# Performance work log

Hardware: AMD Instinct MI355X
Metric: run time of the kernel (lower is better)

The kernel has to match this reference:

```python
import jax, jax.numpy as jnp
import numpy as np

N = 100000   # n_entity
D = 128      # kg_emb_dim
R = 12       # n_relation
NB = 8       # num_bases
E = 1_000_000
P = 400_000  # hypergraph incidences
HE = 20_000  # hyperedges
B = 64       # users in batch
LR = 64      # related entities per hypergraph per user
LC = 32      # context entities per user
NH = 8       # mha heads
HD = D // NH


def setup_inputs() -> dict:
    key = jax.random.key(0)
    ks = jax.random.split(key, 32)
    s = 1.0 / np.sqrt(D)
    f = lambda i, shape, sc=s: jax.random.normal(ks[i], shape, dtype=jnp.float32) * sc
    ri = lambda i, shape, hi: jax.random.randint(ks[i], shape, 0, hi, dtype=jnp.int32)
    return {
        'entity_emb': f(0, (N, D)),
        'rgcn_bases': f(1, (NB, D, D)),
        'rgcn_comp': f(2, (R, NB)),
        'rgcn_root': f(3, (D, D)),
        'rgcn_bias': jnp.zeros((D,), jnp.float32),
        'sess_theta': f(4, (D, D)),
        'sess_bias': jnp.zeros((D,), jnp.float32),
        'know_theta': f(5, (D, D)),
        'know_bias': jnp.zeros((D,), jnp.float32),
        'in_proj_w': f(6, (3 * D, D)),
        'in_proj_b': jnp.zeros((3 * D,), jnp.float32),
        'out_proj_w': f(7, (D, D)),
        'out_proj_b': jnp.zeros((D,), jnp.float32),
        'attn_his_a': f(8, (D, D)),
        'attn_his_b': f(9, (D, 1)),
        'attn_a': f(10, (D, D)),
        'attn_b': f(11, (D, 1)),
        'rec_bias': jnp.zeros((N,), jnp.float32),
        'edge_src': ri(12, (E,), N),
        'edge_dst': ri(13, (E,), N),
        'edge_type': ri(14, (E,), R),
        'sess_nodes': ri(15, (P,), N),
        'sess_edges': ri(16, (P,), HE),
        'know_nodes': ri(17, (P,), N),
        'know_edges': ri(18, (P,), HE),
        'sess_rel_idx': ri(19, (B, LR), N),
        'know_rel_idx': ri(20, (B, LR), N),
        'context_idx': ri(21, (B, LC), N),
    }


def rgcn_conv(x, bases, comp, root, bias, src, dst, etype):
    # PyG RGCNConv with basis decomposition; per-relation mean aggregation
    # norm = 1/|N_r(i)| : count edges per (dst, relation)
    pair_key = dst * R + etype
    cnt = jax.ops.segment_sum(jnp.ones_like(src, dtype=x.dtype), pair_key, N * R)
    norm = 1.0 / jnp.maximum(cnt[pair_key], 1.0)  # [E]
    w = jnp.einsum('rb,bio->rio', comp, bases)    # [R, D, D]
    out = x @ root + bias
    for r in range(R):
        h_r = x @ w[r]                                            # [N, D]
        coef = norm * (etype == r).astype(x.dtype)                # [E]
        out = out + jax.ops.segment_sum(h_r[src] * coef[:, None], dst, N)
    return out


def hypergraph_conv(x, theta, bias, nodes, edges, n_hyperedges):
    # PyG HypergraphConv (no attention): D^-1 H W B^-1 H^T X Theta + bias
    xt = x @ theta                                                # [N, D]
    ones = jnp.ones(nodes.shape, x.dtype)
    b_deg = jax.ops.segment_sum(ones, edges, n_hyperedges)        # [HE]
    edge_feat = jax.ops.segment_sum(xt[nodes], edges, n_hyperedges)
    edge_feat = edge_feat * jnp.where(b_deg > 0, 1.0 / b_deg, 0.0)[:, None]
    d_deg = jax.ops.segment_sum(ones, nodes, N)                   # [N]
    out = jax.ops.segment_sum(edge_feat[edges], nodes, N)
    return out * jnp.where(d_deg > 0, 1.0 / d_deg, 0.0)[:, None] + bias


def self_attn_batch(h, a, b):
    # SelfAttentionBatch: e = tanh(h a) b; softmax over nodes; weighted sum
    e = jnp.einsum('bld,dk->blk', jnp.tanh(jnp.einsum('bld,de->ble', h, a)), b)[..., 0]
    attn = jax.nn.softmax(e, axis=-1)                             # [B, L]
    return jnp.einsum('bl,bld->bd', attn, h)


def mha(q, kv, in_proj_w, in_proj_b, out_proj_w, out_proj_b):
    # torch.nn.MultiheadAttention (batch_first) math
    wq, wk, wv = in_proj_w[:D], in_proj_w[D:2 * D], in_proj_w[2 * D:]
    bq, bk, bv = in_proj_b[:D], in_proj_b[D:2 * D], in_proj_b[2 * D:]
    qh = (q @ wq.T + bq).reshape(q.shape[0], q.shape[1], NH, HD)
    kh = (kv @ wk.T + bk).reshape(kv.shape[0], kv.shape[1], NH, HD)
    vh = (kv @ wv.T + bv).reshape(kv.shape[0], kv.shape[1], NH, HD)
    logits = jnp.einsum('bqhd,bkhd->bhqk', qh, kh) / np.sqrt(HD)
    attn = jax.nn.softmax(logits, axis=-1)
    o = jnp.einsum('bhqk,bkhd->bqhd', attn, vh).reshape(q.shape[0], q.shape[1], D)
    return o @ out_proj_w.T + out_proj_b


def reference(entity_emb, rgcn_bases, rgcn_comp, rgcn_root, rgcn_bias,
              sess_theta, sess_bias, know_theta, know_bias,
              in_proj_w, in_proj_b, out_proj_w, out_proj_b,
              attn_his_a, attn_his_b, attn_a, attn_b, rec_bias,
              edge_src, edge_dst, edge_type,
              sess_nodes, sess_edges, know_nodes, know_edges,
              sess_rel_idx, know_rel_idx, context_idx):
    # 1) RGCN over the full KG
    kg = rgcn_conv(entity_emb, rgcn_bases, rgcn_comp, rgcn_root, rgcn_bias,
                   edge_src, edge_dst, edge_type)
    # 2) session / knowledge hypergraph convolutions on RGCN output
    sess = hypergraph_conv(kg, sess_theta, sess_bias, sess_nodes, sess_edges, HE)
    know = hypergraph_conv(kg, know_theta, know_bias, know_nodes, know_edges, HE)
    # 3) per-user: related = concat(session_emb, knowledge_emb); context from kg
    related = jnp.concatenate([sess[sess_rel_idx], know[know_rel_idx]], axis=1)  # [B, 2LR, D]
    context = kg[context_idx]                                                    # [B, LC, D]
    # 4) MHItemAttention (context queries related) + gated attention pooling
    att_rel = mha(context, related, in_proj_w, in_proj_b, out_proj_w, out_proj_b)
    his = self_attn_batch(att_rel, attn_his_a, attn_his_b)                       # [B, D]
    user_cat = jnp.concatenate([context, his[:, None, :]], axis=1)               # [B, LC+1, D]
    user = self_attn_batch(user_cat, attn_a, attn_b)                             # [B, D]
    # 5) recommendation scores: F.linear(user, kg_embedding, rec_bias.bias)
    return user @ kg.T + rec_bias                                                # [B, N]
```

## Files before the change

kernel.cpp:

```cpp
#include <hip/hip_runtime.h>
#include <hip/hip_bf16.h>

#define DN 100000
#define DD 128
#define DR 12
#define DNB 8
#define DE 1000000
#define DP 400000
#define DHE 20000
#define DHE2 40000
#define DB 64
#define DLR 64
#define DLC 32
#define DNH 8
#define DHD 16
#define NRBINS (DR * DN)
#define NALLBINS (NRBINS + DHE2)
#define SCAN_CHUNK 1024
#define MCAP 65536

typedef unsigned short ushortT;
typedef unsigned int uintT;
typedef __attribute__((ext_vector_type(8))) short s8v;
typedef __attribute__((ext_vector_type(4))) float f4v;

#define APAD 136
#define ASLB 40
#define BSP 40

__device__ __forceinline__ ushortT rneb(float v) {
    uintT b = __float_as_uint(v);
    return (ushortT)((b + 0x7FFFu + ((b >> 16) & 1u)) >> 16);
}
__device__ __forceinline__ float b2f(ushortT h) {
    return __uint_as_float(((uintT)h) << 16);
}

__device__ __forceinline__ void split_store8(ushortT* hbase, ushortT* lbase, const float* v)
{
    ushortT h[8], l[8];
    #pragma unroll
    for (int j = 0; j < 8; ++j) {
        h[j] = rneb(v[j]);
        l[j] = rneb(v[j] - b2f(h[j]));
    }
    uint4 hv = make_uint4((uintT)h[0] | ((uintT)h[1] << 16), (uintT)h[2] | ((uintT)h[3] << 16),
                          (uintT)h[4] | ((uintT)h[5] << 16), (uintT)h[6] | ((uintT)h[7] << 16));
    uint4 lv = make_uint4((uintT)l[0] | ((uintT)l[1] << 16), (uintT)l[2] | ((uintT)l[3] << 16),
                          (uintT)l[4] | ((uintT)l[5] << 16), (uintT)l[6] | ((uintT)l[7] << 16));
    *(uint4*)hbase = hv;
    *(uint4*)lbase = lv;
}

__global__ __launch_bounds__(256) void k_presplit_all(
    const float* __restrict__ root, const float* __restrict__ st,
    const float* __restrict__ kt, const float* __restrict__ ipw,
    const float* __restrict__ opw, const float* __restrict__ aha,
    const float* __restrict__ aa, ushortT* __restrict__ outA)
{
    int gid = blockIdx.x * 256 + threadIdx.x;
    int mat = gid >> 14, e = gid & 16383;
    const float* srcs[9] = {root, st, kt, ipw, ipw + 16384, ipw + 32768, opw, aha, aa};
    const float* W = srcs[mat];
    bool t1 = (mat >= 3 && mat <= 6);
    int k = e & 31, n = (e >> 5) & 127, kc = e >> 12;
    float f = t1 ? W[(size_t)n * 128 + kc * 32 + k] : W[(size_t)(kc * 32 + k) * 128 + n];
    ushortT h = rneb(f);
    outA[(size_t)mat * 32768 + e] = h;
    outA[(size_t)mat * 32768 + 16384 + e] = rneb(f - b2f(h));
}

__global__ void k_wcomp_split(const float* __restrict__ comp, const float* __restrict__ bases,
                              ushortT* __restrict__ warena)
{
    int i = blockIdx.x * blockDim.x + threadIdx.x;
    if (i >= DR * DD * DD) return;
    int r = i / (DD * DD), io = i % (DD * DD);
    float s = 0.f;
    #pragma unroll
    for (int b = 0; b < DNB; ++b) s += comp[r * DNB + b] * bases[(size_t)b * DD * DD + io];
    int irow = io >> 7, o = io & 127;
    int kc = irow >> 5, k = irow & 31;
    size_t dst = (size_t)r * 32768 + (size_t)kc * 4096 + o * 32 + k;
    ushortT h = rneb(s);
    warena[dst] = h;
    warena[dst + 16384] = rneb(s - b2f(h));
}

__global__ __launch_bounds__(256) void k_gemm_ds(
    const float* __restrict__ A, const ushortT* __restrict__ Wb,
    const float* __restrict__ bias, const float* __restrict__ rs,
    const int* __restrict__ gidx, float* __restrict__ gout,
    float* __restrict__ C, int M)
{
    __shared__ __align__(16) ushortT Ah[64 * APAD], Al[64 * APAD];
    __shared__ __align__(16) ushortT Bs[8192];
    int tid = threadIdx.x;
    int row0 = blockIdx.x * 64;
    {
        int row = tid >> 2, c0 = (tid & 3) * 32;
        int gr = row0 + row;
        int arow = gr;
        if (gidx && gr < M) arow = gidx[gr];
        const float* ar = A + (size_t)arow * 128 + c0;
        float sc = 1.0f;
        if (rs && gr < M) { float d = rs[gr]; sc = (d > 0.f) ? 1.0f / d : 0.f; }
        #pragma unroll
        for (int g = 0; g < 4; ++g) {
            float v[8] = {};
            if (gr < M) {
                float4 u0 = *(const float4*)(ar + g * 8);
                float4 u1 = *(const float4*)(ar + g * 8 + 4);
                v[0]=u0.x*sc; v[1]=u0.y*sc; v[2]=u0.z*sc; v[3]=u0.w*sc;
                v[4]=u1.x*sc; v[5]=u1.y*sc; v[6]=u1.z*sc; v[7]=u1.w*sc;
                if (gout) {
                    *(float4*)(gout + (size_t)gr * 128 + c0 + g * 8)     = u0;
                    *(float4*)(gout + (size_t)gr * 128 + c0 + g * 8 + 4) = u1;
                }
            }
            split_store8(&Ah[row * APAD + c0 + g * 8], &Al[row * APAD + c0 + g * 8], v);
        }
    }
    f4v acc[8] = {};
    int w = tid >> 6, lane = tid & 63, m = lane & 15, quad = lane >> 4;
    for (int kc = 0; kc < 4; ++kc) {
        __syncthreads();
        {
            const ushortT* gh = Wb + kc * 4096;
            const ushortT* gl = Wb + 16384 + kc * 4096;
            *(s8v*)&Bs[tid * 8]        = *(const s8v*)&gh[tid * 8];
            *(s8v*)&Bs[2048 + tid * 8] = *(const s8v*)&gh[2048 + tid * 8];
            *(s8v*)&Bs[4096 + tid * 8] = *(const s8v*)&gl[tid * 8];
            *(s8v*)&Bs[6144 + tid * 8] = *(const s8v*)&gl[2048 + tid * 8];
        }
        __syncthreads();
        s8v ah = *(const s8v*)&Ah[(w * 16 + m) * APAD + kc * 32 + quad * 8];
        s8v al = *(const s8v*)&Al[(w * 16 + m) * APAD + kc * 32 + quad * 8];
        #pragma unroll
        for (int nt = 0; nt < 8; ++nt) {
            int boff = (nt * 16 + m) * 32 + quad * 8;
            s8v bh = *(const s8v*)&Bs[boff];
            s8v bl = *(const s8v*)&Bs[4096 + boff];
            acc[nt] = __builtin_amdgcn_mfma_f32_16x16x32_bf16(ah, bh, acc[nt], 0, 0, 0);
            acc[nt] = __builtin_amdgcn_mfma_f32_16x16x32_bf16(al, bh, acc[nt], 0, 0, 0);
            acc[nt] = __builtin_amdgcn_mfma_f32_16x16x32_bf16(ah, bl, acc[nt], 0, 0, 0);
        }
    }
    float bv[8];
    #pragma unroll
    for (int nt = 0; nt < 8; ++nt) bv[nt] = bias ? bias[nt * 16 + m] : 0.f;
    #pragma unroll
    for (int rr = 0; rr < 4; ++rr) {
        int gr = row0 + w * 16 + quad * 4 + rr;
        if (gr < M) {
            #pragma unroll
            for (int nt = 0; nt < 8; ++nt)
                C[(size_t)gr * 128 + nt * 16 + m] = acc[nt][rr] + bv[nt];
        }
    }
}

__global__ __launch_bounds__(256) void k_tanh_dot_ds(
    const float* __restrict__ A, const ushortT* __restrict__ Wb,
    const float* __restrict__ bvec, float* __restrict__ e, int M)
{
    __shared__ __align__(16) ushortT Ah[64 * APAD], Al[64 * APAD];
    __shared__ __align__(16) ushortT Bs[8192];
    int tid = threadIdx.x;
    int row0 = blockIdx.x * 64;
    {
        int row = tid >> 2, c0 = (tid & 3) * 32;
        int gr = row0 + row;
        const float* ar = A + (size_t)gr * 128 + c0;
        #pragma unroll
        for (int g = 0; g < 4; ++g) {
            float v[8] = {};
            if (gr < M) {
                float4 u0 = *(const float4*)(ar + g * 8);
                float4 u1 = *(const float4*)(ar + g * 8 + 4);
                v[0]=u0.x; v[1]=u0.y; v[2]=u0.z; v[3]=u0.w;
                v[4]=u1.x; v[5]=u1.y; v[6]=u1.z; v[7]=u1.w;
            }
            split_store8(&Ah[row * APAD + c0 + g * 8], &Al[row * APAD + c0 + g * 8], v);
        }
    }
    f4v acc[8] = {};
    int w = tid >> 6, lane = tid & 63, m = lane & 15, quad = lane >> 4;
    for (int kc = 0; kc < 4; ++kc) {
        __syncthreads();
        {
            const ushortT* gh = Wb + kc * 4096;
            const ushortT* gl = Wb + 16384 + kc * 4096;
            *(s8v*)&Bs[tid * 8]        = *(const s8v*)&gh[tid * 8];
            *(s8v*)&Bs[2048 + tid * 8] = *(const s8v*)&gh[2048 + tid * 8];
            *(s8v*)&Bs[4096 + tid * 8] = *(const s8v*)&gl[tid * 8];
            *(s8v*)&Bs[6144 + tid * 8] = *(const s8v*)&gl[2048 + tid * 8];
        }
        __syncthreads();
        s8v ah = *(const s8v*)&Ah[(w * 16 + m) * APAD + kc * 32 + quad * 8];
        s8v al = *(const s8v*)&Al[(w * 16 + m) * APAD + kc * 32 + quad * 8];
        #pragma unroll
        for (int nt = 0; nt < 8; ++nt) {
            int boff = (nt * 16 + m) * 32 + quad * 8;
            s8v bh = *(const s8v*)&Bs[boff];
            s8v bl = *(const s8v*)&Bs[4096 + boff];
            acc[nt] = __builtin_amdgcn_mfma_f32_16x16x32_bf16(ah, bh, acc[nt], 0, 0, 0);
            acc[nt] = __builtin_amdgcn_mfma_f32_16x16x32_bf16(al, bh, acc[nt], 0, 0, 0);
            acc[nt] = __builtin_amdgcn_mfma_f32_16x16x32_bf16(ah, bl, acc[nt], 0, 0, 0);
        }
    }
    float bv[8];
    #pragma unroll
    for (int nt = 0; nt < 8; ++nt) bv[nt] = bvec[nt * 16 + m];
    #pragma unroll
    for (int rr = 0; rr < 4; ++rr) {
        float p = 0.f;
        #pragma unroll
        for (int nt = 0; nt < 8; ++nt) p += tanhf(acc[nt][rr]) * bv[nt];
        #pragma unroll
        for (int o = 1; o < 16; o <<= 1) p += __shfl_xor(p, o);
        int gr = row0 + w * 16 + quad * 4 + rr;
        if (m == 0 && gr < M) e[gr] = p;
    }
}

template <int L>
__global__ __launch_bounds__(128) void k_pool_apply(const float* __restrict__ h,
                                                    const float* __restrict__ e,
                                                    float* __restrict__ out,
                                                    ushortT* __restrict__ us)
{
    __shared__ float es[L];
    int b = blockIdx.x, tid = threadIdx.x;
    if (tid < L) es[tid] = e[b * L + tid];
    __syncthreads();
    float mx = -1e30f;
    #pragma unroll
    for (int l = 0; l < L; ++l) mx = fmaxf(mx, es[l]);
    float wgt[L];
    float sum = 0.f;
    #pragma unroll
    for (int l = 0; l < L; ++l) { wgt[l] = __expf(es[l] - mx); sum += wgt[l]; }
    float inv = 1.0f / sum;
    float o = 0.f;
    #pragma unroll
    for (int l = 0; l < L; ++l) o += wgt[l] * h[((size_t)b * L + l) * 128 + tid];
    float val = o * inv;
    out[(size_t)b * 128 + tid] = val;
    if (us) {
        ushortT hh = rneb(val);
        ushortT ll = rneb(val - b2f(hh));
        int e_ = ((tid >> 5) * 2048) + b * 32 + (tid & 31);
        us[e_] = hh;
        us[8192 + e_] = ll;
    }
}

__global__ void k_build_ucat(const float* __restrict__ ctx, const float* __restrict__ his,
                             float* ucat)
{
    int i = blockIdx.x * blockDim.x + threadIdx.x;
    if (i >= DB * 33 * 128) return;
    int d = i & 127, l = (i >> 7) % 33, b = i / (33 * 128);
    ucat[i] = (l < 32) ? ctx[((size_t)b * 32 + l) * 128 + d] : his[(size_t)b * 128 + d];
}

__global__ __launch_bounds__(256) void k_rgcn_fk(
    const float* __restrict__ x, const ushortT* __restrict__ rootsplit,
    const ushortT* __restrict__ warena, const float* __restrict__ bias,
    const int* __restrict__ soff, const int* __restrict__ hist,
    const int* __restrict__ ssrc, float* __restrict__ kg)
{
    __shared__ __align__(16) ushortT Ah[64 * ASLB], Al[64 * ASLB];
    __shared__ __align__(16) ushortT Bs[2 * 128 * BSP];
    int tid = threadIdx.x;
    int dst0 = blockIdx.x * 64;
    int nrow = min(64, DN - dst0);
    int w = tid >> 6, lane = tid & 63, m = lane & 15, quad = lane >> 4;
    int row = tid >> 2, ci = (tid & 3) * 8;
    int brow = tid & 127, bpl = tid >> 7;
    f4v acc[8] = {};

    for (int p = 0; p < 13; ++p) {
        float a[32];
        if (row < nrow) {
            if (p == 0) {
                const float* ar = x + (size_t)(dst0 + row) * 128 + ci;
                #pragma unroll
                for (int k = 0; k < 4; ++k) {
                    float4 u0 = *(const float4*)(ar + k * 32);
                    float4 u1 = *(const float4*)(ar + k * 32 + 4);
                    a[k*8+0]=u0.x; a[k*8+1]=u0.y; a[k*8+2]=u0.z; a[k*8+3]=u0.w;
                    a[k*8+4]=u1.x; a[k*8+5]=u1.y; a[k*8+6]=u1.z; a[k*8+7]=u1.w;
                }
            } else {
                #pragma unroll
                for (int j = 0; j < 32; ++j) a[j] = 0.f;
                int key = (dst0 + row) * DR + (p - 1);
                int len = hist[key];
                int st = soff[key] - len;
                for (int i = 0; i < len; ++i) {
                    const float* xr = x + (size_t)ssrc[st + i] * 128 + ci;
                    #pragma unroll
                    for (int k = 0; k < 4; ++k) {
                        float4 u0 = *(const float4*)(xr + k * 32);
                        float4 u1 = *(const float4*)(xr + k * 32 + 4);
                        a[k*8+0]+=u0.x; a[k*8+1]+=u0.y; a[k*8+2]+=u0.z; a[k*8+3]+=u0.w;
                        a[k*8+4]+=u1.x; a[k*8+5]+=u1.y; a[k*8+6]+=u1.z; a[k*8+7]+=u1.w;
                    }
                }
                float inv = (len > 0) ? 1.0f / (float)len : 0.f;
                #pragma unroll
                for (int j = 0; j < 32; ++j) a[j] *= inv;
            }
        } else {
            #pragma unroll
            for (int j = 0; j < 32; ++j) a[j] = 0.f;
        }
        const ushortT* Wb = (p == 0) ? rootsplit : warena + (size_t)(p - 1) * 32768;
        #pragma unroll
        for (int kci = 0; kci < 4; ++kci) {
            __syncthreads();
            split_store8(&Ah[row * ASLB + ci], &Al[row * ASLB + ci], a + kci * 8);
            {
                const ushortT* src = Wb + bpl * 16384 + kci * 4096 + brow * 32;
                ushortT* dstp = &Bs[bpl * (128 * BSP) + brow * BSP];
                *(s8v*)&dstp[0]  = *(const s8v*)&src[0];
                *(s8v*)&dstp[8]  = *(const s8v*)&src[8];
                *(s8v*)&dstp[16] = *(const s8v*)&src[16];
                *(s8v*)&dstp[24] = *(const s8v*)&src[24];
            }
            __syncthreads();
            s8v ah = *(const s8v*)&Ah[(w * 16 + m) * ASLB + quad * 8];
            s8v al = *(const s8v*)&Al[(w * 16 + m) * ASLB + quad * 8];
            #pragma unroll
            for (int nt = 0; nt < 8; ++nt) {
                int boff = (nt * 16 + m) * BSP + quad * 8;
                s8v bh = *(const s8v*)&Bs[boff];
                s8v bl2 = *(const s8v*)&Bs[128 * BSP + boff];
                acc[nt] = __builtin_amdgcn_mfma_f32_16x16x32_bf16(ah, bh, acc[nt], 0, 0, 0);
                acc[nt] = __builtin_amdgcn_mfma_f32_16x16x32_bf16(al, bh, acc[nt], 0, 0, 0);
                acc[nt] = __builtin_amdgcn_mfma_f32_16x16x32_bf16(ah, bl2, acc[nt], 0, 0, 0);
            }
        }
    }
    float bv[8];
    #pragma unroll
    for (int nt = 0; nt < 8; ++nt) bv[nt] = bias[nt * 16 + m];
    #pragma unroll
    for (int rr = 0; rr < 4; ++rr) {
        int gr = dst0 + w * 16 + quad * 4 + rr;
        if (gr < DN) {
            #pragma unroll
            for (int nt = 0; nt < 8; ++nt)
                kg[(size_t)gr * 128 + nt * 16 + m] = acc[nt][rr] + bv[nt];
        }
    }
}

__global__ __launch_bounds__(256) void k_score_ds(
    const float* __restrict__ kg, const ushortT* __restrict__ Ub,
    const float* __restrict__ rb, float* __restrict__ out)
{
    __shared__ __align__(16) ushortT Ah[64 * APAD], Al[64 * APAD];
    __shared__ __align__(16) ushortT Bs[4096];
    int tid = threadIdx.x;
    int n0 = blockIdx.x * 64;
    {
        int row = tid >> 2, c0 = (tid & 3) * 32;
        int gr = n0 + row;
        const float* ar = kg + (size_t)gr * 128 + c0;
        #pragma unroll
        for (int g = 0; g < 4; ++g) {
            float v[8] = {};
            if (gr < DN) {
                float4 u0 = *(const float4*)(ar + g * 8);
                float4 u1 = *(const float4*)(ar + g * 8 + 4);
                v[0]=u0.x; v[1]=u0.y; v[2]=u0.z; v[3]=u0.w;
                v[4]=u1.x; v[5]=u1.y; v[6]=u1.z; v[7]=u1.w;
            }
            split_store8(&Ah[row * APAD + c0 + g * 8], &Al[row * APAD + c0 + g * 8], v);
        }
    }
    f4v acc[4] = {};
    int w = tid >> 6, lane = tid & 63, m = lane & 15, quad = lane >> 4;
    for (int kc = 0; kc < 4; ++kc) {
        __syncthreads();
        {
            const ushortT* gh = Ub + kc * 2048;
            const ushortT* gl = Ub + 8192 + kc * 2048;
            *(s8v*)&Bs[tid * 8]        = *(const s8v*)&gh[tid * 8];
            *(s8v*)&Bs[2048 + tid * 8] = *(const s8v*)&gl[tid * 8];
        }
        __syncthreads();
        s8v ah = *(const s8v*)&Ah[(w * 16 + m) * APAD + kc * 32 + quad * 8];
        s8v al = *(const s8v*)&Al[(w * 16 + m) * APAD + kc * 32 + quad * 8];
        #pragma unroll
        for (int nt = 0; nt < 4; ++nt) {
            int boff = (nt * 16 + m) * 32 + quad * 8;
            s8v bh = *(const s8v*)&Bs[boff];
            s8v bl = *(const s8v*)&Bs[2048 + boff];
            acc[nt] = __builtin_amdgcn_mfma_f32_16x16x32_bf16(ah, bh, acc[nt], 0, 0, 0);
            acc[nt] = __builtin_amdgcn_mfma_f32_16x16x32_bf16(al, bh, acc[nt], 0, 0, 0);
            acc[nt] = __builtin_amdgcn_mfma_f32_16x16x32_bf16(ah, bl, acc[nt], 0, 0, 0);
        }
    }
    int n = n0 + w * 16 + quad * 4;
    if (n < DN) {
        float4 rbv = *(const float4*)&rb[n];
        #pragma unroll
        for (int nt = 0; nt < 4; ++nt) {
            int b = nt * 16 + m;
            float4 o = make_float4(acc[nt][0] + rbv.x, acc[nt][1] + rbv.y,
                                   acc[nt][2] + rbv.z, acc[nt][3] + rbv.w);
            *(float4*)&out[(size_t)b * DN + n] = o;
        }
    }
}

__global__ void k_scan_pass1(const int* __restrict__ in, int n, int* __restrict__ bsum)
{
    __shared__ int red[256];
    int b = blockIdx.x, t = threadIdx.x;
    int i0 = b * SCAN_CHUNK + t * 4;
    int s = 0;
    #pragma unroll
    for (int j = 0; j < 4; ++j) {
        int i = i0 + j;
        if (i < n) s += in[i];
    }
    red[t] = s;
    __syncthreads();
    for (int o = 128; o > 0; o >>= 1) {
        if (t < o) red[t] += red[t + o];
        __syncthreads();
    }
    if (t == 0) bsum[b] = red[0];
}

__global__ __launch_bounds__(256) void k_scan_pass2p(int* bsum, int nb, int* total)
{
    __shared__ int lds[256];
    __shared__ int carry;
    int t = threadIdx.x;
    if (t == 0) carry = 0;
    __syncthreads();
    for (int c0 = 0; c0 < nb; c0 += 256) {
        int i = c0 + t;
        int v = (i < nb) ? bsum[i] : 0;
        lds[t] = v;
        __syncthreads();
        for (int o = 1; o < 256; o <<= 1) {
            int add = (t >= o) ? lds[t - o] : 0;
            __syncthreads();
            lds[t] += add;
            __syncthreads();
        }
        int myc = carry;
        if (i < nb) bsum[i] = lds[t] - v + myc;
        int tot = lds[255];
        __syncthreads();
        if (t == 0) carry = myc + tot;
        __syncthreads();
    }
    if (total && t == 0) *total = carry;
}

__global__ void k_scan_pass3(const int* __restrict__ in, int n, const int* __restrict__ bsum,
                             int* __restrict__ out)
{
    __shared__ int lds[256];
    int b = blockIdx.x, t = threadIdx.x;
    int i0 = b * SCAN_CHUNK + t * 4;
    int v[4]; int s = 0;
    #pragma unroll
    for (int j = 0; j < 4; ++j) {
        int i = i0 + j;
        int x = 0;
        if (i < n) x = in[i];
        v[j] = x; s += x;
    }
    lds[t] = s;
    __syncthreads();
    for (int o = 1; o < 256; o <<= 1) {
        int add = (t >= o) ? lds[t - o] : 0;
        __syncthreads();
        lds[t] += add;
        __syncthreads();
    }
    int run = lds[t] - s + bsum[b];
    #pragma unroll
    for (int j = 0; j < 4; ++j) {
        int i = i0 + j;
        if (i < n) { out[i] = run; run += v[j]; }
    }
}

__global__ void k_hist_both(const int* __restrict__ dst, const int* __restrict__ et,
                            int* __restrict__ hist,
                            const int* __restrict__ se, const int* __restrict__ ke)
{
    int i = blockIdx.x * blockDim.x + threadIdx.x;
    if (i < DE) {
        atomicAdd(&hist[dst[i] * DR + et[i]], 1);
    } else {
        int j = i - DE;
        if (j < DP) atomicAdd(&hist[NRBINS + se[j]], 1);
        else if (j < 2 * DP) atomicAdd(&hist[NRBINS + DHE + ke[j - DP]], 1);
    }
}

__global__ void k_bucket_both(const int* __restrict__ src, const int* __restrict__ dst,
                              const int* __restrict__ et, int* __restrict__ soff,
                              int* __restrict__ ssrc,
                              const int* __restrict__ sn, const int* __restrict__ se,
                              const int* __restrict__ kn, const int* __restrict__ ke,
                              int* __restrict__ pns)
{
    int i = blockIdx.x * blockDim.x + threadIdx.x;
    if (i < DE) {
        int key = dst[i] * DR + et[i];
        int pos = atomicAdd(&soff[key], 1);
        ssrc[pos] = src[i];
    } else {
        int j = i - DE;
        if (j >= 2 * DP) return;
        int e, node;
        if (j < DP) { e = se[j]; node = sn[j]; }
        else { e = DHE + ke[j - DP]; node = kn[j - DP]; }
        int pos = atomicAdd(&soff[NRBINS + e], 1);
        pns[pos - DE] = node;
    }
}

__global__ void k_hyper_agg(const float* __restrict__ xsrc, const int* __restrict__ pns,
                            const int* __restrict__ hoff, const int* __restrict__ hcnt,
                            const int* __restrict__ heneed, float* __restrict__ efeat)
{
    int lane = threadIdx.x & 63;
    int he = (blockIdx.x * blockDim.x + threadIdx.x) >> 6;
    if (he >= DHE2) return;
    if (!heneed[he]) return;
    int len = hcnt[he];
    int st = hoff[he] - len - DE;
    int half = lane >> 5;
    int c16 = (lane & 31) * 4;
    float4 acc = make_float4(0.f, 0.f, 0.f, 0.f);
    int c = 0;
    for (; c + 4 <= len; c += 4) {
        int n0 = pns[st + c + half];
        int n1 = pns[st + c + 2 + half];
        float4 v0 = *(const float4*)&xsrc[(size_t)n0 * 128 + c16];
        float4 v1 = *(const float4*)&xsrc[(size_t)n1 * 128 + c16];
        acc.x += v0.x + v1.x; acc.y += v0.y + v1.y;
        acc.z += v0.z + v1.z; acc.w += v0.w + v1.w;
    }
    for (; c < len; c += 2) {
        int idx = c + half;
        if (idx < len) {
            int n = pns[st + idx];
            float4 v = *(const float4*)&xsrc[(size_t)n * 128 + c16];
            acc.x += v.x; acc.y += v.y; acc.z += v.z; acc.w += v.w;
        }
    }
    acc.x += __shfl_xor(acc.x, 32);
    acc.y += __shfl_xor(acc.y, 32);
    acc.z += __shfl_xor(acc.z, 32);
    acc.w += __shfl_xor(acc.w, 32);
    if (half == 0) {
        float inv = (len > 0) ? 1.0f / (float)len : 0.f;
        float4 o = make_float4(acc.x * inv, acc.y * inv, acc.z * inv, acc.w * inv);
        *(float4*)&efeat[(size_t)he * 128 + c16] = o;
    }
}

__global__ void k_slot_assign2(const int* __restrict__ sidx, const int* __restrict__ kidx,
                               int* slot_s, int* slot_k, int* scnt)
{
    int i = blockIdx.x * blockDim.x + threadIdx.x;
    if (i < DB * DLR) {
        int node = sidx[i];
        if (atomicCAS(&slot_s[node], -1, -2) == -1) slot_s[node] = atomicAdd(&scnt[0], 1);
    } else if (i < 2 * DB * DLR) {
        int node = kidx[i - DB * DLR];
        if (atomicCAS(&slot_k[node], -1, -2) == -1) slot_k[node] = atomicAdd(&scnt[1], 1);
    }
}

__global__ __launch_bounds__(256) void k_sdeg_match(
    const int* __restrict__ nodes, const int* __restrict__ he, const int* __restrict__ slot,
    float* sdeg, int* mcnt, int* mhe, int* msl, int* heneed, int heBase)
{
    __shared__ int lcnt, lbase;
    if (threadIdx.x == 0) lcnt = 0;
    __syncthreads();
    int i = blockIdx.x * 256 + threadIdx.x;
    int s = -1, lidx = 0, h = 0;
    if (i < DP) {
        s = slot[nodes[i]];
        if (s >= 0) {
            h = heBase + he[i];
            heneed[h] = 1;
            atomicAdd(&sdeg[s], 1.0f);
            lidx = atomicAdd(&lcnt, 1);
        }
    }
    __syncthreads();
    if (threadIdx.x == 0) lbase = (lcnt > 0) ? atomicAdd(mcnt, lcnt) : 0;
    __syncthreads();
    if (s >= 0) {
        int idx = lbase + lidx;
        if (idx < MCAP) { mhe[idx] = h; msl[idx] = s; }
    }
}

__global__ void k_accmatch2(const float* __restrict__ efeat,
                            const int* __restrict__ mhe_s, const int* __restrict__ msl_s,
                            const int* __restrict__ mhe_k, const int* __restrict__ msl_k,
                            const int* __restrict__ mcnt,
                            float* sacc_s, float* sacc_k)
{
    int lane = threadIdx.x & 63;
    int w = (blockIdx.x * blockDim.x + threadIdx.x) >> 6;
    int nw = (gridDim.x * blockDim.x) >> 6;
    int Ms = min(mcnt[0], MCAP), Mk = min(mcnt[1], MCAP);
    for (int i = w; i < Ms + Mk; i += nw) {
        bool sess = i < Ms;
        int he = sess ? mhe_s[i] : mhe_k[i - Ms];
        int sl = sess ? msl_s[i] : msl_k[i - Ms];
        float* sacc = sess ? sacc_s : sacc_k;
        float2 v = *(const float2*)&efeat[(size_t)he * 128 + lane * 2];
        atomicAdd(&sacc[(size_t)sl * 128 + lane * 2],     v.x);
        atomicAdd(&sacc[(size_t)sl * 128 + lane * 2 + 1], v.y);
    }
}

__global__ void k_rel_gather2(const float* __restrict__ so_s, const float* __restrict__ so_k,
                              const int* __restrict__ slot_s, const int* __restrict__ slot_k,
                              const int* __restrict__ ridx_s, const int* __restrict__ ridx_k,
                              float* __restrict__ related)
{
    int gid = blockIdx.x * blockDim.x + threadIdx.x;
    int i = gid >> 5, c = gid & 31;
    if (i >= 2 * DB * DLR) return;
    bool sess = i < DB * DLR;
    int ii = sess ? i : i - DB * DLR;
    int s = sess ? slot_s[ridx_s[ii]] : slot_k[ridx_k[ii]];
    const float* so = sess ? so_s : so_k;
    int b = ii / DLR, l = ii % DLR;
    int colOff = sess ? 0 : 64;
    ((float4*)&related[((size_t)b * 128 + colOff + l) * 128])[c] =
        ((const float4*)&so[(size_t)s * 128])[c];
}

__global__ __launch_bounds__(256) void k_mha(const float* __restrict__ qb,
                                             const float* __restrict__ kb,
                                             const float* __restrict__ vb,
                                             float* __restrict__ ob)
{
    int b = blockIdx.x >> 3, h = blockIdx.x & 7;
    __shared__ float Ks[128][16], Vs[128][16], Qs[32][16];
    int tid = threadIdx.x;
    for (int i = tid; i < 128 * 16; i += 256) {
        int j = i >> 4, d = i & 15;
        Ks[j][d] = kb[((size_t)b * 128 + j) * 128 + h * 16 + d];
        Vs[j][d] = vb[((size_t)b * 128 + j) * 128 + h * 16 + d];
    }
    for (int i = tid; i < 32 * 16; i += 256) {
        int q = i >> 4, d = i & 15;
        Qs[q][d] = qb[((size_t)b * 32 + q) * 128 + h * 16 + d] * 0.25f;
    }
    __syncthreads();
    int q = tid >> 3;
    int jg = tid & 7;
    float lg[16];
    float m = -1e30f;
    #pragma unroll
    for (int jj = 0; jj < 16; ++jj) {
        int j = jg * 16 + jj;
        float s = 0.f;
        #pragma unroll
        for (int d = 0; d < 16; ++d) s += Qs[q][d] * Ks[j][d];
        lg[jj] = s;
        m = fmaxf(m, s);
    }
    #pragma unroll
    for (int o = 1; o < 8; o <<= 1) m = fmaxf(m, __shfl_xor(m, o));
    float sum = 0.f;
    float acc[16] = {};
    #pragma unroll
    for (int jj = 0; jj < 16; ++jj) {
        float p = __expf(lg[jj] - m);
        sum += p;
        int j = jg * 16 + jj;
        #pragma unroll
        for (int d = 0; d < 16; ++d) acc[d] += p * Vs[j][d];
    }
    #pragma unroll
    for (int o = 1; o < 8; o <<= 1) {
        sum += __shfl_xor(sum, o);
        #pragma unroll
        for (int d = 0; d < 16; ++d) acc[d] += __shfl_xor(acc[d], o);
    }
    if (jg == 0) {
        float inv = 1.0f / sum;
        #pragma unroll
        for (int d = 0; d < 16; ++d)
            ob[((size_t)b * 32 + q) * 128 + h * 16 + d] = acc[d] * inv;
    }
}

extern "C" void kernel_launch(void* const* d_in, const int* in_sizes, int n_in,
                              void* d_out, int out_size, void* d_ws, size_t ws_size,
                              hipStream_t stream)
{
    const float* emb        = (const float*)d_in[0];
    const float* bases      = (const float*)d_in[1];
    const float* comp       = (const float*)d_in[2];
    const float* root       = (const float*)d_in[3];
    const float* rgcn_bias  = (const float*)d_in[4];
    const float* sess_theta = (const float*)d_in[5];
    const float* sess_bias  = (const float*)d_in[6];
    const float* know_theta = (const float*)d_in[7];
    const float* know_bias  = (const float*)d_in[8];
    const float* in_proj_w  = (const float*)d_in[9];
    const float* in_proj_b  = (const float*)d_in[10];
    const float* out_proj_w = (const float*)d_in[11];
    const float* out_proj_b = (const float*)d_in[12];
    const float* attn_his_a = (const float*)d_in[13];
    const float* attn_his_b = (const float*)d_in[14];
    const float* attn_a     = (const float*)d_in[15];
    const float* attn_b     = (const float*)d_in[16];
    const float* rec_bias   = (const float*)d_in[17];
    const int* edge_src     = (const int*)d_in[18];
    const int* edge_dst     = (const int*)d_in[19];
    const int* edge_type    = (const int*)d_in[20];
    const int* sess_nodes   = (const int*)d_in[21];
    const int* sess_edges   = (const int*)d_in[22];
    const int* know_nodes   = (const int*)d_in[23];
    const int* know_edges   = (const int*)d_in[24];
    const int* sess_rel_idx = (const int*)d_in[25];
    const int* know_rel_idx = (const int*)d_in[26];
    const int* context_idx  = (const int*)d_in[27];
    float* out = (float*)d_out;

    float* wsf = (float*)d_ws;
    size_t off = 0;
    auto alloc = [&](size_t n) { size_t r = off; off += (n + 255) & ~(size_t)255; return r; };
    float* kg      = wsf + alloc(12800000);
    float* tmp     = wsf + alloc(12800000);
    ushortT* warena = (ushortT*)(wsf + alloc(196608));
    int*   bsumV   = (int*)(wsf + alloc(2048));
    size_t zstart = off;
    int*   heneed  = (int*)(wsf + alloc(DHE2));
    int*   mcnt    = (int*)(wsf + alloc(16));
    int*   scnt    = (int*)(wsf + alloc(16));
    float* sdeg_s  = wsf + alloc(4096);
    float* sdeg_k  = wsf + alloc(4096);
    float* sacc_s  = wsf + alloc(524288);
    float* sacc_k  = wsf + alloc(524288);
    size_t zend = off;
    size_t fstart = off;
    int*   slot_s  = (int*)(wsf + alloc(100000));
    int*   slot_k  = (int*)(wsf + alloc(100000));
    size_t fend = off;
    int*   pns     = (int*)(wsf + alloc(2 * DP));
    int*   mhe_s   = (int*)(wsf + alloc(MCAP));
    int*   msl_s   = (int*)(wsf + alloc(MCAP));
    int*   mhe_k   = (int*)(wsf + alloc(MCAP));
    int*   msl_k   = (int*)(wsf + alloc(MCAP));
    float* so_s    = wsf + alloc(524288);
    float* so_k    = wsf + alloc(524288);
    float* related = wsf + alloc(1048576);
    float* ctx     = wsf + alloc(262144);
    float* qb      = wsf + alloc(262144);
    float* kb      = wsf + alloc(1048576);
    float* vb      = wsf + alloc(1048576);
    float* obuf    = wsf + alloc(262144);
    float* attrel  = wsf + alloc(262144);
    float* his     = wsf + alloc(8192);
    float* ucat    = wsf + alloc(270336);
    float* userb   = wsf + alloc(8192);
    float* e1      = wsf + alloc(2048);
    float* e2      = wsf + alloc(2112);
    (void)ws_size; (void)in_sizes; (void)n_in; (void)out_size;

    int*   hist    = (int*)tmp;
    int*   soff    = (int*)tmp + 1240000;
    int*   ssrc    = (int*)tmp + 2480000;
    float* efeat   = tmp + 3600000;
    ushortT* wsplit = (ushortT*)(tmp + 12200000);
    ushortT* usplit = (ushortT*)(tmp + 12400000);

    const int nbA = (NALLBINS + SCAN_CHUNK - 1) / SCAN_CHUNK;

    hipMemsetAsync(wsf + zstart, 0, (zend - zstart) * 4, stream);
    hipMemsetAsync(wsf + fstart, 0xFF, (fend - fstart) * 4, stream);
    hipMemsetAsync(hist, 0, (size_t)NALLBINS * 4, stream);

    k_presplit_all<<<576, 256, 0, stream>>>(root, sess_theta, know_theta, in_proj_w,
                                            out_proj_w, attn_his_a, attn_a, wsplit);

    k_slot_assign2<<<32, 256, 0, stream>>>(sess_rel_idx, know_rel_idx, slot_s, slot_k, scnt);
    k_sdeg_match<<<(DP + 255) / 256, 256, 0, stream>>>(sess_nodes, sess_edges, slot_s,
                                                       sdeg_s, mcnt, mhe_s, msl_s, heneed, 0);
    k_sdeg_match<<<(DP + 255) / 256, 256, 0, stream>>>(know_nodes, know_edges, slot_k,
                                                       sdeg_k, mcnt + 1, mhe_k, msl_k, heneed, DHE);

    k_hist_both<<<(DE + 2 * DP + 255) / 256, 256, 0, stream>>>(edge_dst, edge_type, hist,
                                                               sess_edges, know_edges);
    k_scan_pass1<<<nbA, 256, 0, stream>>>(hist, NALLBINS, bsumV);
    k_scan_pass2p<<<1, 256, 0, stream>>>(bsumV, nbA, nullptr);
    k_scan_pass3<<<nbA, 256, 0, stream>>>(hist, NALLBINS, bsumV, soff);
    k_bucket_both<<<(DE + 2 * DP + 255) / 256, 256, 0, stream>>>(
        edge_src, edge_dst, edge_type, soff, ssrc,
        sess_nodes, sess_edges, know_nodes, know_edges, pns);

    k_wcomp_split<<<(DR * DD * DD + 255) / 256, 256, 0, stream>>>(comp, bases, warena);

    int gemmN = (DN + 63) / 64;
    k_rgcn_fk<<<gemmN, 256, 0, stream>>>(emb, wsplit + 0 * 32768, warena, rgcn_bias,
                                         soff, hist, ssrc, kg);

    k_hyper_agg<<<(DHE2 * 64 + 255) / 256, 256, 0, stream>>>(kg, pns, soff + NRBINS,
                                                             hist + NRBINS, heneed, efeat);
    k_accmatch2<<<256, 256, 0, stream>>>(efeat, mhe_s, msl_s, mhe_k, msl_k, mcnt, sacc_s, sacc_k);

    k_gemm_ds<<<64, 256, 0, stream>>>(sacc_s, wsplit + 1 * 32768, sess_bias, sdeg_s,
                                      nullptr, nullptr, so_s, 4096);
    k_gemm_ds<<<64, 256, 0, stream>>>(sacc_k, wsplit + 2 * 32768, know_bias, sdeg_k,
                                      nullptr, nullptr, so_k, 4096);
    k_rel_gather2<<<(2 * DB * DLR * 32 + 255) / 256, 256, 0, stream>>>(
        so_s, so_k, slot_s, slot_k, sess_rel_idx, know_rel_idx, related);

    k_gemm_ds<<<(DB * DLC + 63) / 64, 256, 0, stream>>>(kg, wsplit + 3 * 32768,
                                                        in_proj_b, nullptr,
                                                        context_idx, ctx, qb, DB * DLC);
    k_gemm_ds<<<(DB * 128 + 63) / 64, 256, 0, stream>>>(related, wsplit + 4 * 32768,
                                                        in_proj_b + DD, nullptr,
                                                        nullptr, nullptr, kb, DB * 128);
    k_gemm_ds<<<(DB * 128 + 63) / 64, 256, 0, stream>>>(related, wsplit + 5 * 32768,
                                                        in_proj_b + 2 * DD, nullptr,
                                                        nullptr, nullptr, vb, DB * 128);
    k_mha<<<DB * DNH, 256, 0, stream>>>(qb, kb, vb, obuf);
    k_gemm_ds<<<(DB * DLC + 63) / 64, 256, 0, stream>>>(obuf, wsplit + 6 * 32768,
                                                        out_proj_b, nullptr,
                                                        nullptr, nullptr, attrel, DB * DLC);

    k_tanh_dot_ds<<<(DB * DLC + 63) / 64, 256, 0, stream>>>(attrel, wsplit + 7 * 32768,
                                                            attn_his_b, e1, DB * DLC);
    k_pool_apply<32><<<DB, 128, 0, stream>>>(attrel, e1, his, nullptr);
    k_build_ucat<<<(DB * 33 * 128 + 255) / 256, 256, 0, stream>>>(ctx, his, ucat);
    k_tanh_dot_ds<<<(DB * 33 + 63) / 64, 256, 0, stream>>>(ucat, wsplit + 8 * 32768,
                                                           attn_b, e2, DB * 33);
    k_pool_apply<33><<<DB, 128, 0, stream>>>(ucat, e2, userb, usplit);
    k_score_ds<<<gemmN, 256, 0, stream>>>(kg, usplit, rec_bias, out);
}
```

Measured before the change: 806.4 us.

## Keep RGCN A fragments in registers and double-buffer weight tiles with prefetch

The fused RGCN kernel no longer stages the gathered and mean-aggregated activations through shared memory. Each lane gathers exactly the row and columns it needs for its MFMA A fragment and splits them into bf16 hi/lo in registers. Weight tiles are prefetched into registers one step ahead and written to a double-buffered shared tile, cutting barriers to one per k-step and overlapping the global weight loads with MFMA work. The neighbour-gather loop is also unrolled by two to put more loads in flight, at the cost of higher register pressure.

```diff
diff --git a/kernel.cpp b/kernel.cpp
--- a/kernel.cpp
+++ b/kernel.cpp
@@ -25,8 +25,8 @@
 typedef __attribute__((ext_vector_type(4))) float f4v;
 
 #define APAD 136
-#define ASLB 40
 #define BSP 40
+#define BUFO (2 * 128 * BSP)
 
 __device__ __forceinline__ ushortT rneb(float v) {
     uintT b = __float_as_uint(v);
@@ -50,6 +50,19 @@
                           (uintT)l[4] | ((uintT)l[5] << 16), (uintT)l[6] | ((uintT)l[7] << 16));
     *(uint4*)hbase = hv;
     *(uint4*)lbase = lv;
+}
+
+__device__ __forceinline__ void split_pack8(const float* v, s8v* hv, s8v* lv)
+{
+    s8v h, l;
+    #pragma unroll
+    for (int j = 0; j < 8; ++j) {
+        ushortT hh = rneb(v[j]);
+        h[j] = (short)hh;
+        l[j] = (short)rneb(v[j] - b2f(hh));
+    }
+    *hv = h;
+    *lv = l;
 }
 
 __global__ __launch_bounds__(256) void k_presplit_all(
@@ -271,77 +284,104 @@
     const int* __restrict__ soff, const int* __restrict__ hist,
     const int* __restrict__ ssrc, float* __restrict__ kg)
 {
-    __shared__ __align__(16) ushortT Ah[64 * ASLB], Al[64 * ASLB];
-    __shared__ __align__(16) ushortT Bs[2 * 128 * BSP];
+    __shared__ __align__(16) ushortT Bs[2 * BUFO];
     int tid = threadIdx.x;
     int dst0 = blockIdx.x * 64;
-    int nrow = min(64, DN - dst0);
     int w = tid >> 6, lane = tid & 63, m = lane & 15, quad = lane >> 4;
-    int row = tid >> 2, ci = (tid & 3) * 8;
+    int gr = dst0 + w * 16 + m;
+    int ci = quad * 8;
+    bool rowok = (gr < DN);
     int brow = tid & 127, bpl = tid >> 7;
     f4v acc[8] = {};
-
-    for (int p = 0; p < 13; ++p) {
-        float a[32];
-        if (row < nrow) {
-            if (p == 0) {
-                const float* ar = x + (size_t)(dst0 + row) * 128 + ci;
-                #pragma unroll
-                for (int k = 0; k < 4; ++k) {
-                    float4 u0 = *(const float4*)(ar + k * 32);
-                    float4 u1 = *(const float4*)(ar + k * 32 + 4);
-                    a[k*8+0]=u0.x; a[k*8+1]=u0.y; a[k*8+2]=u0.z; a[k*8+3]=u0.w;
-                    a[k*8+4]=u1.x; a[k*8+5]=u1.y; a[k*8+6]=u1.z; a[k*8+7]=u1.w;
+    s8v br0, br1, br2, br3;
+
+    {
+        const ushortT* src = rootsplit + bpl * 16384 + brow * 32;
+        br0 = *(const s8v*)&src[0];  br1 = *(const s8v*)&src[8];
+        br2 = *(const s8v*)&src[16]; br3 = *(const s8v*)&src[24];
+        ushortT* d = &Bs[bpl * (128 * BSP) + brow * BSP];
+        *(s8v*)&d[0] = br0;  *(s8v*)&d[8] = br1;
+        *(s8v*)&d[16] = br2; *(s8v*)&d[24] = br3;
+    }
+    float a[32];
+    for (int s = 0; s < 52; ++s) {
+        int p = s >> 2, kci = s & 3;
+        if (s < 51) {
+            int sn = s + 1, pn = sn >> 2, kcn = sn & 3;
+            const ushortT* Wn = (pn == 0) ? rootsplit : warena + (size_t)(pn - 1) * 32768;
+            const ushortT* src = Wn + bpl * 16384 + kcn * 4096 + brow * 32;
+            br0 = *(const s8v*)&src[0];  br1 = *(const s8v*)&src[8];
+            br2 = *(const s8v*)&src[16]; br3 = *(const s8v*)&src[24];
+        }
+        if (kci == 0) {
+            if (rowok) {
+                if (p == 0) {
+                    const float* ar = x + (size_t)gr * 128 + ci;
+                    #pragma unroll
+                    for (int k = 0; k < 4; ++k) {
+                        float4 u0 = *(const float4*)(ar + k * 32);
+                        float4 u1 = *(const float4*)(ar + k * 32 + 4);
+                        a[k*8+0]=u0.x; a[k*8+1]=u0.y; a[k*8+2]=u0.z; a[k*8+3]=u0.w;
+                        a[k*8+4]=u1.x; a[k*8+5]=u1.y; a[k*8+6]=u1.z; a[k*8+7]=u1.w;
+                    }
+                } else {
+                    #pragma unroll
+                    for (int j = 0; j < 32; ++j) a[j] = 0.f;
+                    int key = gr * DR + (p - 1);
+                    int len = hist[key];
+                    int st = soff[key] - len;
+                    int i = 0;
+                    for (; i + 2 <= len; i += 2) {
+                        const float* x0 = x + (size_t)ssrc[st + i] * 128 + ci;
+                        const float* x1 = x + (size_t)ssrc[st + i + 1] * 128 + ci;
+                        #pragma unroll
+                        for (int k = 0; k < 4; ++k) {
+                            float4 u0 = *(const float4*)(x0 + k * 32);
+                            float4 u1 = *(const float4*)(x0 + k * 32 + 4);
+                            float4 v0 = *(const float4*)(x1 + k * 32);
+                            float4 v1 = *(const float4*)(x1 + k * 32 + 4);
+                            a[k*8+0]+=u0.x+v0.x; a[k*8+1]+=u0.y+v0.y;
+                            a[k*8+2]+=u0.z+v0.z; a[k*8+3]+=u0.w+v0.w;
+                            a[k*8+4]+=u1.x+v1.x; a[k*8+5]+=u1.y+v1.y;
+                            a[k*8+6]+=u1.z+v1.z; a[k*8+7]+=u1.w+v1.w;
+                        }
+                    }
+                    if (i < len) {
+                        const float* x0 = x + (size_t)ssrc[st + i] * 128 + ci;
+                        #pragma unroll
+                        for (int k = 0; k < 4; ++k) {
+                            float4 u0 = *(const float4*)(x0 + k * 32);
+                            float4 u1 = *(const float4*)(x0 + k * 32 + 4);
+                            a[k*8+0]+=u0.x; a[k*8+1]+=u0.y; a[k*8+2]+=u0.z; a[k*8+3]+=u0.w;
+                            a[k*8+4]+=u1.x; a[k*8+5]+=u1.y; a[k*8+6]+=u1.z; a[k*8+7]+=u1.w;
+                        }
+                    }
+                    float inv = (len > 0) ? 1.0f / (float)len : 0.f;
+                    #pragma unroll
+                    for (int j = 0; j < 32; ++j) a[j] *= inv;
                 }
             } else {
                 #pragma unroll
                 for (int j = 0; j < 32; ++j) a[j] = 0.f;
-                int key = (dst0 + row) * DR + (p - 1);
-                int len = hist[key];
-                int st = soff[key] - len;
-                for (int i = 0; i < len; ++i) {
-                    const float* xr = x + (size_t)ssrc[st + i] * 128 + ci;
-                    #pragma unroll
-                    for (int k = 0; k < 4; ++k) {
-                        float4 u0 = *(const float4*)(xr + k * 32);
-                        float4 u1 = *(const float4*)(xr + k * 32 + 4);
-                        a[k*8+0]+=u0.x; a[k*8+1]+=u0.y; a[k*8+2]+=u0.z; a[k*8+3]+=u0.w;
-                        a[k*8+4]+=u1.x; a[k*8+5]+=u1.y; a[k*8+6]+=u1.z; a[k*8+7]+=u1.w;
-                    }
-                }
-                float inv = (len > 0) ? 1.0f / (float)len : 0.f;
-                #pragma unroll
-                for (int j = 0; j < 32; ++j) a[j] *= inv;
             }
-        } else {
-            #pragma unroll
-            for (int j = 0; j < 32; ++j) a[j] = 0.f;
-        }
-        const ushortT* Wb = (p == 0) ? rootsplit : warena + (size_t)(p - 1) * 32768;
-        #pragma unroll
-        for (int kci = 0; kci < 4; ++kci) {
-            __syncthreads();
-            split_store8(&Ah[row * ASLB + ci], &Al[row * ASLB + ci], a + kci * 8);
-            {
-                const ushortT* src = Wb + bpl * 16384 + kci * 4096 + brow * 32;
-                ushortT* dstp = &Bs[bpl * (128 * BSP) + brow * BSP];
-                *(s8v*)&dstp[0]  = *(const s8v*)&src[0];
-                *(s8v*)&dstp[8]  = *(const s8v*)&src[8];
-                *(s8v*)&dstp[16] = *(const s8v*)&src[16];
-                *(s8v*)&dstp[24] = *(const s8v*)&src[24];
-            }
-            __syncthreads();
-            s8v ah = *(const s8v*)&Ah[(w * 16 + m) * ASLB + quad * 8];
-            s8v al = *(const s8v*)&Al[(w * 16 + m) * ASLB + quad * 8];
-            #pragma unroll
-            for (int nt = 0; nt < 8; ++nt) {
-                int boff = (nt * 16 + m) * BSP + quad * 8;
-                s8v bh = *(const s8v*)&Bs[boff];
-                s8v bl2 = *(const s8v*)&Bs[128 * BSP + boff];
-                acc[nt] = __builtin_amdgcn_mfma_f32_16x16x32_bf16(ah, bh, acc[nt], 0, 0, 0);
-                acc[nt] = __builtin_amdgcn_mfma_f32_16x16x32_bf16(al, bh, acc[nt], 0, 0, 0);
-                acc[nt] = __builtin_amdgcn_mfma_f32_16x16x32_bf16(ah, bl2, acc[nt], 0, 0, 0);
-            }
+        }
+        __syncthreads();
+        int bufo = (s & 1) * BUFO;
+        s8v ah, al;
+        split_pack8(a + kci * 8, &ah, &al);
+        #pragma unroll
+        for (int nt = 0; nt < 8; ++nt) {
+            int boff = bufo + (nt * 16 + m) * BSP + quad * 8;
+            s8v bh = *(const s8v*)&Bs[boff];
+            s8v bl2 = *(const s8v*)&Bs[boff + 128 * BSP];
+            acc[nt] = __builtin_amdgcn_mfma_f32_16x16x32_bf16(ah, bh, acc[nt], 0, 0, 0);
+            acc[nt] = __builtin_amdgcn_mfma_f32_16x16x32_bf16(al, bh, acc[nt], 0, 0, 0);
+            acc[nt] = __builtin_amdgcn_mfma_f32_16x16x32_bf16(ah, bl2, acc[nt], 0, 0, 0);
+        }
+        if (s < 51) {
+            ushortT* d = &Bs[((s + 1) & 1) * BUFO + bpl * (128 * BSP) + brow * BSP];
+            *(s8v*)&d[0] = br0;  *(s8v*)&d[8] = br1;
+            *(s8v*)&d[16] = br2; *(s8v*)&d[24] = br3;
         }
     }
     float bv[8];
@@ -349,11 +389,11 @@
     for (int nt = 0; nt < 8; ++nt) bv[nt] = bias[nt * 16 + m];
     #pragma unroll
     for (int rr = 0; rr < 4; ++rr) {
-        int gr = dst0 + w * 16 + quad * 4 + rr;
-        if (gr < DN) {
+        int go = dst0 + w * 16 + quad * 4 + rr;
+        if (go < DN) {
             #pragma unroll
             for (int nt = 0; nt < 8; ++nt)
-                kg[(size_t)gr * 128 + nt * 16 + m] = acc[nt][rr] + bv[nt];
+                kg[(size_t)go * 128 + nt * 16 + m] = acc[nt][rr] + bv[nt];
         }
     }
 }
```

Result: slower. 846.4 us (+5.0%).
